# Kernel tuning notes

Measured on AMD Instinct MI355X. Metric: run time of the kernel, lower is better.

The kernel has to match this reference:

```python
import jax, jax.numpy as jnp
import numpy as np

B, L, D = 64, 512, 768          # batch, BERT seq len, BERT hidden
J = 31                          # clause boundaries per doc
S = J + 1                       # clauses per doc (= decoder max_len)
H = 100                         # enc/dec GRU hidden
NC = 10                         # num label classes
EMB = 50                        # label embedding dim


def setup_inputs() -> dict:
    key = jax.random.key(0)
    ks = jax.random.split(key, 24)
    sc = 0.05
    hidden_state = jax.random.normal(ks[0], (B, L, D), jnp.float32)
    # strictly increasing, non-zero boundaries -> every clause slice is non-empty
    stride = L // S  # 16
    bert_clause_b = jnp.tile(((jnp.arange(J) + 1) * stride)[None, :], (B, 1)).astype(jnp.int32)
    p = dict(
        hidden_state=hidden_state,
        bert_clause_b=bert_clause_b,
        fc5_w=sc * jax.random.normal(ks[1], (D, 1), jnp.float32),
        fc5_b=jnp.zeros((1,), jnp.float32),
        # encoder bi-GRU (input 768 -> hidden 100), torch gate order r,z,n
        enc_wih_f=sc * jax.random.normal(ks[2], (3 * H, D), jnp.float32),
        enc_whh_f=sc * jax.random.normal(ks[3], (3 * H, H), jnp.float32),
        enc_bih_f=jnp.zeros((3 * H,), jnp.float32),
        enc_bhh_f=jnp.zeros((3 * H,), jnp.float32),
        enc_wih_b=sc * jax.random.normal(ks[4], (3 * H, D), jnp.float32),
        enc_whh_b=sc * jax.random.normal(ks[5], (3 * H, H), jnp.float32),
        enc_bih_b=jnp.zeros((3 * H,), jnp.float32),
        enc_bhh_b=jnp.zeros((3 * H,), jnp.float32),
        emb=sc * jax.random.normal(ks[6], (NC, EMB), jnp.float32),
        lin1_w=sc * jax.random.normal(ks[7], (H, 2 * H), jnp.float32),
        lin1_b=jnp.zeros((H,), jnp.float32),
        dec_wih=sc * jax.random.normal(ks[8], (3 * H, EMB + H), jnp.float32),
        dec_whh=sc * jax.random.normal(ks[9], (3 * H, H), jnp.float32),
        dec_bih=jnp.zeros((3 * H,), jnp.float32),
        dec_bhh=jnp.zeros((3 * H,), jnp.float32),
        h2l_w=sc * jax.random.normal(ks[10], (NC, H), jnp.float32),
        h2l_b=jnp.zeros((NC,), jnp.float32),
    )
    return p


def _gru_cell(x, h, wih, whh, bih, bhh):
    gi = x @ wih.T + bih
    gh = h @ whh.T + bhh
    gir, giz, gin = jnp.split(gi, 3, axis=-1)
    ghr, ghz, ghn = jnp.split(gh, 3, axis=-1)
    r = jax.nn.sigmoid(gir + ghr)
    z = jax.nn.sigmoid(giz + ghz)
    n = jnp.tanh(gin + r * ghn)
    return (1.0 - z) * n + z * h


def _gru_scan(xs, h0, wih, whh, bih, bhh):
    # xs: [T, B, I]
    def step(h, x):
        h2 = _gru_cell(x, h, wih, whh, bih, bhh)
        return h2, h2
    return jax.lax.scan(step, h0, xs)


def reference(hidden_state, bert_clause_b, fc5_w, fc5_b,
              enc_wih_f, enc_whh_f, enc_bih_f, enc_bhh_f,
              enc_wih_b, enc_whh_b, enc_bih_b, enc_bhh_b,
              emb, lin1_w, lin1_b, dec_wih, dec_whh, dec_bih, dec_bhh,
              h2l_w, h2l_b):
    # ---- batched_index_select: per-clause softmax-weighted pooling ----
    t = jnp.arange(L)
    seg_id = jnp.sum(t[None, :, None] >= bert_clause_b[:, None, :], axis=-1)  # [B, L]
    scores = jnp.squeeze(hidden_state @ fc5_w, -1) + fc5_b[0]                  # [B, L]
    mask = seg_id[:, None, :] == jnp.arange(S)[None, :, None]                  # [B, S, L]
    logits = jnp.where(mask, scores[:, None, :], -jnp.inf)
    w = jax.nn.softmax(logits, axis=-1)                                        # [B, S, L]
    doc = jnp.einsum('bsl,bld->bsd', w, hidden_state)                          # [B, S, D]

    # ---- encoder bi-GRU ----
    xs = doc.transpose(1, 0, 2)  # [S, B, D]
    h0 = jnp.zeros((B, H), jnp.float32)
    hT_f, ys_f = _gru_scan(xs, h0, enc_wih_f, enc_whh_f, enc_bih_f, enc_bhh_f)
    _, ys_b = _gru_scan(xs[::-1], h0, enc_wih_b, enc_whh_b, enc_bih_b, enc_bhh_b)
    output1 = jnp.concatenate([ys_f, ys_b[::-1]], axis=-1)  # [S, B, 2H]

    # ---- decoder (greedy / testing=True path) ----
    lin = output1 @ lin1_w.T + lin1_b  # [S, B, H]

    def dec_step(carry, lin_t):
        h, prev = carry
        x = jnp.concatenate([emb[prev], lin_t], axis=-1)  # [B, EMB+H]
        h2 = _gru_cell(x, h, dec_wih, dec_whh, dec_bih, dec_bhh)
        logp = jax.nn.log_softmax(h2 @ h2l_w.T + h2l_b, axis=-1)  # [B, NC]
        nxt = jnp.argmax(logp, axis=-1).astype(jnp.int32)
        return (h2, nxt), logp

    init = (hT_f, jnp.zeros((B,), jnp.int32))
    _, outputs = jax.lax.scan(dec_step, init, lin)
    return outputs  # [S, B, NC] log-probs
```

## Files before the change

kernel.cpp:

```cpp
#include <hip/hip_runtime.h>
#include <hip/hip_bf16.h>
#include <math.h>

#define B_ 64
#define L_ 512
#define D_ 768
#define J_ 31
#define S_ 32
#define H_ 100
#define G3 300
#define NC_ 10
#define EMB_ 50
#define OP_ 224

__device__ __forceinline__ float sigmoidf_(float x) { return 1.0f / (1.0f + __expf(-x)); }
__device__ __forceinline__ float tanhf_(float x) {
    float e = __expf(2.0f * x);
    return 1.0f - 2.0f / (e + 1.0f);
}
__device__ __forceinline__ float dot4f_(float4 a, float4 b) {
    return a.x * b.x + a.y * b.y + a.z * b.z + a.w * b.w;
}

typedef _Float16 half2_t __attribute__((ext_vector_type(2)));
typedef _Float16 f16x8 __attribute__((ext_vector_type(8)));
typedef float f32x4 __attribute__((ext_vector_type(4)));
__device__ __forceinline__ half2_t u_as_h2(unsigned u) { return __builtin_bit_cast(half2_t, u); }
__device__ __forceinline__ unsigned packh2(float a, float b) {
    half2_t p; p.x = (_Float16)a; p.y = (_Float16)b;
    return __builtin_bit_cast(unsigned, p);
}

__global__ __launch_bounds__(256) void pool_prep_kernel(
    const float* __restrict__ hs, const int* __restrict__ cb,
    const float* __restrict__ fc5w, const float* __restrict__ fc5b,
    _Float16* __restrict__ doc_h,
    const float* __restrict__ dwih, const float* __restrict__ l1w,
    const float* __restrict__ l1b, const float* __restrict__ emb,
    const float* __restrict__ bih,
    _Float16* __restrict__ W2h, float* __restrict__ b2, float* __restrict__ tcg,
    const float* __restrict__ ewhf, const float* __restrict__ ewhb,
    const float* __restrict__ dwhh, unsigned* __restrict__ wpack,
    const float* __restrict__ ewif, const float* __restrict__ ewib,
    _Float16* __restrict__ wh, _Float16* __restrict__ out1h)
{
    __shared__ __align__(16) float acc_s[4][D_];
    __shared__ float m_s[4], l_s[4];

    int bidx = blockIdx.x;
    int tid = threadIdx.x;

    if (bidx >= 2048) {
        if (bidx < 2348) {
            int n = bidx - 2048;
            __shared__ float dw_s[H_];
            int k = tid;
            if (k < H_) dw_s[k] = dwih[(size_t)n * 150 + 50 + k];
            __syncthreads();
            if (k < 200) {
                float acc = 0.f;
                for (int i = 0; i < H_; ++i) acc += dw_s[i] * l1w[(size_t)i * 200 + k];
                W2h[(size_t)n * OP_ + k] = (_Float16)acc;
            } else if (k == 200) {
                float acc = 0.f;
                for (int i = 0; i < H_; ++i) acc += dw_s[i] * l1b[i];
                b2[n] = acc;
            } else if (k < 211) {
                int c = k - 201;
                float acc = bih[n];
                const float* er = emb + c * EMB_;
                const float* wr = dwih + (size_t)n * 150;
                for (int e = 0; e < EMB_; ++e) acc += er[e] * wr[e];
                tcg[c * G3 + n] = acc;
            } else if (k < 235) {
                W2h[(size_t)n * OP_ + (k - 11)] = (_Float16)0.f;
            }
        } else if (bidx < 2351) {
            int m = bidx - 2348;
            const float* whh = (m == 0) ? ewhf : (m == 1) ? ewhb : dwhh;
            for (int t = tid; t < 400; t += 256) {
                int j = t >> 2, q = t & 3;
                unsigned* o = wpack + (size_t)m * 16000 + (size_t)t * 40;
#pragma unroll
                for (int d = 0; d < 13; ++d) {
                    int k = 2 * (13 * q + d);
                    float r0 = (k < H_) ? whh[j * H_ + k] : 0.f;
                    float r1 = (k + 1 < H_) ? whh[j * H_ + k + 1] : 0.f;
                    float z0 = (k < H_) ? whh[(100 + j) * H_ + k] : 0.f;
                    float z1 = (k + 1 < H_) ? whh[(100 + j) * H_ + k + 1] : 0.f;
                    float n0 = (k < H_) ? whh[(200 + j) * H_ + k] : 0.f;
                    float n1 = (k + 1 < H_) ? whh[(200 + j) * H_ + k + 1] : 0.f;
                    o[d]      = packh2(r0, r1);
                    o[13 + d] = packh2(z0, z1);
                    o[26 + d] = packh2(n0, n1);
                }
                o[39] = 0u;
            }
        } else if (bidx < 2503) {
            int ri = bidx - 2351;
            for (int idx = tid; idx < 3072; idx += 256) {
                int rr = idx / 768;
                int k = idx - rr * 768;
                int n = 4 * ri + rr;
                float v = 0.f;
                if (n < G3) v = ewif[(size_t)n * D_ + k];
                else if (n < 600) v = ewib[(size_t)(n - G3) * D_ + k];
                wh[(size_t)n * D_ + k] = (_Float16)v;
            }
        } else if (bidx < 2511) {
            int r0 = (bidx - 2503) * 256 + tid;
            _Float16* row = out1h + (size_t)r0 * OP_;
            for (int c = 200; c < OP_; ++c) row[c] = (_Float16)0.f;
        } else {
            for (int idx = tid; idx < 4 * OP_; idx += 256) {
                int r = 300 + idx / OP_, c = idx % OP_;
                W2h[(size_t)r * OP_ + c] = (_Float16)0.f;
            }
        }
        return;
    }

    int s = bidx >> 6, b = bidx & 63;
    int start = (s == 0) ? 0 : cb[b * J_ + s - 1];
    int end   = (s == J_) ? L_ : cb[b * J_ + s];
    int nt = end - start;
    int lane = tid & 63, wv = tid >> 6;

    if (nt <= 0) {
        for (int d = tid; d < D_; d += 256) doc_h[((size_t)s * B_ + b) * D_ + d] = (_Float16)0.f;
        return;
    }

    float4 fwv[3];
#pragma unroll
    for (int i = 0; i < 3; ++i)
        fwv[i] = *(const float4*)(fc5w + 4 * lane + 256 * i);
    float bias = fc5b[0];

    const float* base = hs + ((size_t)b * L_ + start) * D_;
    float m = -INFINITY, l = 0.f;
    float4 acc[3];
#pragma unroll
    for (int i = 0; i < 3; ++i) acc[i] = make_float4(0.f, 0.f, 0.f, 0.f);

    for (int t = wv; t < nt; t += 4) {
        const float* row = base + (size_t)t * D_;
        float4 x0 = *(const float4*)(row + 4 * lane);
        float4 x1 = *(const float4*)(row + 4 * lane + 256);
        float4 x2 = *(const float4*)(row + 4 * lane + 512);
        float p = dot4f_(x0, fwv[0]) + dot4f_(x1, fwv[1]) + dot4f_(x2, fwv[2]);
#pragma unroll
        for (int off = 32; off; off >>= 1) p += __shfl_xor(p, off);
        p += bias;
        if (p > m) {
            float sc = __expf(m - p);
            l *= sc;
#pragma unroll
            for (int i = 0; i < 3; ++i) {
                acc[i].x *= sc; acc[i].y *= sc; acc[i].z *= sc; acc[i].w *= sc;
            }
            m = p;
        }
        float e = __expf(p - m);
        l += e;
        acc[0].x += e * x0.x; acc[0].y += e * x0.y; acc[0].z += e * x0.z; acc[0].w += e * x0.w;
        acc[1].x += e * x1.x; acc[1].y += e * x1.y; acc[1].z += e * x1.z; acc[1].w += e * x1.w;
        acc[2].x += e * x2.x; acc[2].y += e * x2.y; acc[2].z += e * x2.z; acc[2].w += e * x2.w;
    }
#pragma unroll
    for (int i = 0; i < 3; ++i)
        *(float4*)&acc_s[wv][4 * lane + 256 * i] = acc[i];
    if (lane == 0) { m_s[wv] = m; l_s[wv] = l; }
    __syncthreads();

    float M = fmaxf(fmaxf(m_s[0], m_s[1]), fmaxf(m_s[2], m_s[3]));
    float f0 = (l_s[0] > 0.f) ? __expf(m_s[0] - M) : 0.f;
    float f1 = (l_s[1] > 0.f) ? __expf(m_s[1] - M) : 0.f;
    float f2 = (l_s[2] > 0.f) ? __expf(m_s[2] - M) : 0.f;
    float f3 = (l_s[3] > 0.f) ? __expf(m_s[3] - M) : 0.f;
    float inv = 1.f / (l_s[0] * f0 + l_s[1] * f1 + l_s[2] * f2 + l_s[3] * f3);
    _Float16* o = doc_h + ((size_t)s * B_ + b) * D_;
#pragma unroll
    for (int i = 0; i < 3; ++i) {
        int d = tid + 256 * i;
        float num = acc_s[0][d] * f0 + acc_s[1][d] * f1
                  + acc_s[2][d] * f2 + acc_s[3][d] * f3;
        o[d] = (_Float16)(num * inv);
    }
}

__global__ __launch_bounds__(256) void gemm_enc_mfma(
    const _Float16* __restrict__ dh, const _Float16* __restrict__ wh,
    const float* __restrict__ bf_, const float* __restrict__ bb_,
    float* __restrict__ C)
{
    int w = threadIdx.x >> 6, l = threadIdx.x & 63;
    int m0 = (blockIdx.y * 4 + w) * 16;
    int n0 = blockIdx.x * 16;
    int rowA = m0 + (l & 15);
    int rowB = n0 + (l & 15);
    int kb = (l >> 4) * 8;

    const f16x8* ap = (const f16x8*)(dh + (size_t)rowA * D_ + kb);
    const f16x8* bp = (const f16x8*)(wh + (size_t)rowB * D_ + kb);
    f32x4 acc = {0.f, 0.f, 0.f, 0.f};
#pragma unroll
    for (int k = 0; k < 24; ++k) {
        f16x8 a = ap[k * 4];
        f16x8 b = bp[k * 4];
        acc = __builtin_amdgcn_mfma_f32_16x16x32_f16(a, b, acc, 0, 0, 0);
    }
    int nc = n0 + (l & 15);
    if (nc < 600) {
        float bias = (nc < G3) ? bf_[nc] : bb_[nc - G3];
#pragma unroll
        for (int r = 0; r < 4; ++r) {
            int mr = m0 + (l >> 4) * 4 + r;
            C[(size_t)mr * 600 + nc] = acc[r] + bias;
        }
    }
}

__global__ __launch_bounds__(256) void gemm_gil_mfma(
    const _Float16* __restrict__ oh, const _Float16* __restrict__ W2h,
    const float* __restrict__ b2, float* __restrict__ C)
{
    int w = threadIdx.x >> 6, l = threadIdx.x & 63;
    int m0 = (blockIdx.y * 4 + w) * 16;
    int n0 = blockIdx.x * 16;
    const f16x8* ap = (const f16x8*)(oh + (size_t)(m0 + (l & 15)) * OP_ + (l >> 4) * 8);
    const f16x8* bp = (const f16x8*)(W2h + (size_t)(n0 + (l & 15)) * OP_ + (l >> 4) * 8);
    f32x4 acc = {0.f, 0.f, 0.f, 0.f};
#pragma unroll
    for (int k = 0; k < 7; ++k) {
        f16x8 a = ap[k * 4];
        f16x8 b = bp[k * 4];
        acc = __builtin_amdgcn_mfma_f32_16x16x32_f16(a, b, acc, 0, 0, 0);
    }
    int nc = n0 + (l & 15);
    if (nc < G3) {
        float bias = b2[nc];
#pragma unroll
        for (int r = 0; r < 4; ++r) {
            int mr = m0 + (l >> 4) * 4 + r;
            C[(size_t)mr * G3 + nc] = acc[r] + bias;
        }
    }
}

#define LOAD_WREGS(WPBASE)                                                  \
    uint4 wq[10];                                                           \
    if (mv) {                                                               \
        const uint4* wp_ = (const uint4*)((WPBASE) + (size_t)tid * 40);     \
        _Pragma("unroll")                                                   \
        for (int i = 0; i < 10; ++i) wq[i] = wp_[i];                        \
    }

#define WD(i) (((i) & 3) == 0 ? wq[(i) >> 2].x : ((i) & 3) == 1 ? wq[(i) >> 2].y \
             : ((i) & 3) == 2 ? wq[(i) >> 2].z : wq[(i) >> 2].w)

#define MATVEC_REG(PBUF)                                                    \
    {                                                                       \
        const unsigned* hh = (const unsigned*)(PBUF);                       \
        _Pragma("unroll")                                                   \
        for (int d = 0; d < 13; ++d) {                                      \
            half2_t hv = u_as_h2(hh[13 * q + d]);                           \
            ar = __builtin_amdgcn_fdot2(u_as_h2(WD(d)),      hv, ar, false); \
            az = __builtin_amdgcn_fdot2(u_as_h2(WD(13 + d)), hv, az, false); \
            an = __builtin_amdgcn_fdot2(u_as_h2(WD(26 + d)), hv, an, false); \
        }                                                                   \
        ar += __shfl_xor(ar, 1); ar += __shfl_xor(ar, 2);                   \
        az += __shfl_xor(az, 1); az += __shfl_xor(az, 2);                   \
        an += __shfl_xor(an, 1); an += __shfl_xor(an, 2);                   \
    }

#define ENCT 448
#define ENC_SUB(GA0, GA1, GA2, NB0, NB1, NB2, SC, SN)                       \
    {                                                                       \
        if (mv) {                                                           \
            if (q == 0 && (SN) < S_) {                                      \
                int tn_ = bwd ? (S_ - 1 - (SN)) : (SN);                     \
                const float* gg_ = gi + ((size_t)tn_ * B_ + b) * 600 + goff; \
                NB0 = gg_[j]; NB1 = gg_[100 + j]; NB2 = gg_[200 + j];       \
            }                                                               \
            float ar = 0.f, az = 0.f, an = 0.f;                             \
            MATVEC_REG(hhalf[p])                                            \
            if (q == 0) {                                                   \
                int tc_ = bwd ? (S_ - 1 - (SC)) : (SC);                     \
                float r = sigmoidf_(GA0 + ar + bhr);                        \
                float z = sigmoidf_(GA1 + az + bhz);                        \
                float n = tanhf_(GA2 + r * (an + bhn));                     \
                float hn = (1.f - z) * n + z * hc;                          \
                hc = hn;                                                    \
                hhalf[p ^ 1][j] = (_Float16)hn;                             \
                out1h[((size_t)tc_ * B_ + b) * OP_ + ooff + j] = (_Float16)hn; \
            }                                                               \
        }                                                                   \
        __syncthreads();                                                    \
        p ^= 1;                                                             \
    }

__global__ __launch_bounds__(ENCT, 1) void enc_scan(
    const float* __restrict__ gi, const unsigned* __restrict__ wpack,
    const float* __restrict__ bhh_f, const float* __restrict__ bhh_b,
    _Float16* __restrict__ out1h, float* __restrict__ hT)
{
    __shared__ __align__(8) _Float16 hhalf[2][104];

    int bid = blockIdx.x;
    int b = bid & 63;
    bool bwd = (bid >= 64);
    const float* bhh = bwd ? bhh_b : bhh_f;
    int tid = threadIdx.x;
    int j = tid >> 2, q = tid & 3;
    bool mv = tid < 400;
    const int goff = bwd ? G3 : 0;
    const int ooff = bwd ? H_ : 0;

    if (tid < 104) { hhalf[0][tid] = (_Float16)0.f; hhalf[1][tid] = (_Float16)0.f; }
    LOAD_WREGS(wpack + (bwd ? 16000 : 0))
    float bhr = 0.f, bhz = 0.f, bhn = 0.f, hc = 0.f;
    float pA0 = 0.f, pA1 = 0.f, pA2 = 0.f, pB0 = 0.f, pB1 = 0.f, pB2 = 0.f;
    if (mv && q == 0) {
        bhr = bhh[j]; bhz = bhh[100 + j]; bhn = bhh[200 + j];
        int t0 = bwd ? (S_ - 1) : 0;
        const float* gg = gi + ((size_t)t0 * B_ + b) * 600 + goff;
        pA0 = gg[j]; pA1 = gg[100 + j]; pA2 = gg[200 + j];
    }
    __syncthreads();

    int p = 0;
    for (int step = 0; step < S_; step += 2) {
        ENC_SUB(pA0, pA1, pA2, pB0, pB1, pB2, step, step + 1)
        ENC_SUB(pB0, pB1, pB2, pA0, pA1, pA2, step + 1, step + 2)
    }
    if (!bwd && mv && q == 0) hT[b * H_ + j] = hc;
}

#define DECT 448
#define DEC_LOGITS(TPREV)                                                   \
    {                                                                       \
        float acc_ = 0.f;                                                   \
        if (lane < 40) {                                                    \
            int c_ = lane >> 2, part_ = lane & 3;                           \
            const float* hr_ = hl_s + c_ * H_;                              \
            const float* hv_ = hf[p];                                       \
            int k0_ = 25 * part_;                                           \
            for (int k_ = k0_; k_ < k0_ + 25; ++k_) acc_ += hr_[k_] * hv_[k_]; \
            acc_ += __shfl_xor(acc_, 1);                                    \
            acc_ += __shfl_xor(acc_, 2);                                    \
        }                                                                   \
        float src_ = __shfl(acc_, (lane < NC_) ? 4 * lane : 0);             \
        float lv_ = (lane < NC_) ? src_ + hlb_r : -INFINITY;                \
        float mx_ = lv_; int am_ = lane & 15;                               \
        _Pragma("unroll")                                                   \
        for (int m_ = 8; m_; m_ >>= 1) {                                    \
            float ov_ = __shfl_xor(mx_, m_);                                \
            int oa_ = __shfl_xor(am_, m_);                                  \
            if (ov_ > mx_ || (ov_ == mx_ && oa_ < am_)) { mx_ = ov_; am_ = oa_; } \
        }                                                                   \
        if (w0) {                                                           \
            float e_ = (lane < NC_) ? __expf(lv_ - mx_) : 0.f;              \
            float se_ = e_;                                                 \
            _Pragma("unroll")                                               \
            for (int m_ = 8; m_; m_ >>= 1) se_ += __shfl_xor(se_, m_);      \
            if (lane < NC_) {                                               \
                float lse_ = mx_ + __logf(se_);                             \
                out[((size_t)(TPREV) * B_ + b) * NC_ + lane] = lv_ - lse_;  \
            }                                                               \
        }                                                                   \
        prev = __shfl(am_, 0);                                              \
    }

#define DEC_SUB(GA0, GA1, GA2, NB0, NB1, NB2, TC)                           \
    {                                                                       \
        float ar = 0.f, az = 0.f, an = 0.f;                                 \
        if (mv && (TC) < S_) {                                              \
            if (q == 0 && (TC) + 1 < S_) {                                  \
                const float* gg_ = gi_lin + ((size_t)((TC) + 1) * B_ + b) * G3; \
                NB0 = gg_[j]; NB1 = gg_[100 + j]; NB2 = gg_[200 + j];       \
            }                                                               \
            MATVEC_REG(hhalf[p])                                            \
        }                                                                   \
        if ((TC) >= 1) DEC_LOGITS((TC) - 1)                                 \
        if (mv && (TC) < S_ && q == 0) {                                    \
            const float* tcp_ = tc_s + prev * G3;                           \
            float r = sigmoidf_(GA0 + tcp_[j]       + ar + bhr);            \
            float z = sigmoidf_(GA1 + tcp_[100 + j] + az + bhz);            \
            float n = tanhf_(   GA2 + tcp_[200 + j] + r * (an + bhn));      \
            float hn = (1.f - z) * n + z * hc;                              \
            hc = hn;                                                        \
            hf[p ^ 1][j] = hn;                                              \
            hhalf[p ^ 1][j] = (_Float16)hn;                                 \
        }                                                                   \
        __syncthreads();                                                    \
        p ^= 1;                                                             \
    }

__global__ __launch_bounds__(DECT, 1) void dec_scan(
    const float* __restrict__ gi_lin, const unsigned* __restrict__ wpack,
    const float* __restrict__ bhh, const float* __restrict__ tcg,
    const float* __restrict__ h2lw, const float* __restrict__ h2lb,
    const float* __restrict__ hT, float* __restrict__ out)
{
    __shared__ float tc_s[NC_ * G3];
    __shared__ float hl_s[NC_ * H_];
    __shared__ __align__(8) _Float16 hhalf[2][104];
    __shared__ __align__(16) float hf[2][104];

    int bid = blockIdx.x;
    int b = bid & 63;
    int tid = threadIdx.x;
    int j = tid >> 2, q = tid & 3;
    bool mv = tid < 400;
    int lane = tid & 63;
    bool w0 = (tid < 64);

    for (int idx = tid; idx < NC_ * G3; idx += DECT) tc_s[idx] = tcg[idx];
    for (int idx = tid; idx < NC_ * H_; idx += DECT) hl_s[idx] = h2lw[idx];
    if (tid < 104) {
        float hv = (tid < H_) ? hT[b * H_ + tid] : 0.f;
        hf[0][tid] = hv;            hf[1][tid] = 0.f;
        hhalf[0][tid] = (_Float16)hv; hhalf[1][tid] = (_Float16)0.f;
    }
    LOAD_WREGS(wpack + 32000)
    float bhr = 0.f, bhz = 0.f, bhn = 0.f, hc = 0.f;
    float pA0 = 0.f, pA1 = 0.f, pA2 = 0.f, pB0 = 0.f, pB1 = 0.f, pB2 = 0.f;
    if (mv && q == 0) {
        bhr = bhh[j]; bhz = bhh[100 + j]; bhn = bhh[200 + j];
        hc = hT[b * H_ + j];
        const float* gg = gi_lin + ((size_t)0 * B_ + b) * G3;
        pA0 = gg[j]; pA1 = gg[100 + j]; pA2 = gg[200 + j];
    }
    float hlb_r = (lane < NC_) ? h2lb[lane] : 0.f;
    int prev = 0;
    __syncthreads();

    int p = 0;
    DEC_SUB(pA0, pA1, pA2, pB0, pB1, pB2, 0)
    for (int it = 0; it < 16; ++it) {
        int tA = 2 * it + 1, tB = 2 * it + 2;
        DEC_SUB(pB0, pB1, pB2, pA0, pA1, pA2, tA)
        DEC_SUB(pA0, pA1, pA2, pB0, pB1, pB2, tB)
    }
}

extern "C" void kernel_launch(void* const* d_in, const int* in_sizes, int n_in,
                              void* d_out, int out_size, void* d_ws, size_t ws_size,
                              hipStream_t stream)
{
    const float* hs   = (const float*)d_in[0];
    const int*   cb   = (const int*)  d_in[1];
    const float* fc5w = (const float*)d_in[2];
    const float* fc5b = (const float*)d_in[3];
    const float* ewif = (const float*)d_in[4];
    const float* ewhf = (const float*)d_in[5];
    const float* ebif = (const float*)d_in[6];
    const float* ebhf = (const float*)d_in[7];
    const float* ewib = (const float*)d_in[8];
    const float* ewhb = (const float*)d_in[9];
    const float* ebib = (const float*)d_in[10];
    const float* ebhb = (const float*)d_in[11];
    const float* emb  = (const float*)d_in[12];
    const float* l1w  = (const float*)d_in[13];
    const float* l1b  = (const float*)d_in[14];
    const float* dwih = (const float*)d_in[15];
    const float* dwhh = (const float*)d_in[16];
    const float* dbih = (const float*)d_in[17];
    const float* dbhh = (const float*)d_in[18];
    const float* h2lw = (const float*)d_in[19];
    const float* h2lb = (const float*)d_in[20];
    float* out = (float*)d_out;

    float* ws   = (float*)d_ws;
    _Float16* doc_h = (_Float16*)ws;
    _Float16* wh    = (_Float16*)(ws + 800000);
    float* gi    = ws + 1572864;
    _Float16* out1h = (_Float16*)(gi + 1228800);
    float* hT    = gi + 1228800 + 230000;
    float* b2    = hT + 6400;
    float* tcg   = b2 + 320;
    float* gil   = tcg + 3072;
    unsigned* wpack = (unsigned*)(gil + 614400);
    _Float16* W2h = (_Float16*)(wpack + 48000);

    pool_prep_kernel<<<2512, 256, 0, stream>>>(
        hs, cb, fc5w, fc5b, doc_h,
        dwih, l1w, l1b, emb, dbih, W2h, b2, tcg,
        ewhf, ewhb, dwhh, wpack,
        ewif, ewib, wh, out1h);
    gemm_enc_mfma<<<dim3(38, 32), 256, 0, stream>>>(doc_h, wh, ebif, ebib, gi);
    enc_scan<<<128, ENCT, 0, stream>>>(gi, wpack, ebhf, ebhb, out1h, hT);
    gemm_gil_mfma<<<dim3(19, 32), 256, 0, stream>>>(out1h, W2h, b2, gil);
    dec_scan<<<64, DECT, 0, stream>>>(gil, wpack, dbhh, tcg,
                                      h2lw, h2lb, hT, out);
}
```

Measured before the change: 144.2 us.

## Fuse input-projection GEMMs into encoder and decoder scan kernels via shared memory

Removes the two standalone MFMA GEMM kernels. Each scan block now computes its own per-batch input projections (32 timesteps by 300 gates) with MFMA into shared memory before the recurrence. This cuts two kernel launches and the global round trip of the gi/gil intermediates. In exchange, the per-batch GEMM runs on only 128 or 64 blocks instead of a wide grid, which makes the scan prologue longer, and the software prefetch of gate inputs is replaced by shared-memory reads.

```diff
diff --git a/kernel.cpp b/kernel.cpp
--- a/kernel.cpp
+++ b/kernel.cpp
@@ -189,65 +189,6 @@
     }
 }
 
-__global__ __launch_bounds__(256) void gemm_enc_mfma(
-    const _Float16* __restrict__ dh, const _Float16* __restrict__ wh,
-    const float* __restrict__ bf_, const float* __restrict__ bb_,
-    float* __restrict__ C)
-{
-    int w = threadIdx.x >> 6, l = threadIdx.x & 63;
-    int m0 = (blockIdx.y * 4 + w) * 16;
-    int n0 = blockIdx.x * 16;
-    int rowA = m0 + (l & 15);
-    int rowB = n0 + (l & 15);
-    int kb = (l >> 4) * 8;
-
-    const f16x8* ap = (const f16x8*)(dh + (size_t)rowA * D_ + kb);
-    const f16x8* bp = (const f16x8*)(wh + (size_t)rowB * D_ + kb);
-    f32x4 acc = {0.f, 0.f, 0.f, 0.f};
-#pragma unroll
-    for (int k = 0; k < 24; ++k) {
-        f16x8 a = ap[k * 4];
-        f16x8 b = bp[k * 4];
-        acc = __builtin_amdgcn_mfma_f32_16x16x32_f16(a, b, acc, 0, 0, 0);
-    }
-    int nc = n0 + (l & 15);
-    if (nc < 600) {
-        float bias = (nc < G3) ? bf_[nc] : bb_[nc - G3];
-#pragma unroll
-        for (int r = 0; r < 4; ++r) {
-            int mr = m0 + (l >> 4) * 4 + r;
-            C[(size_t)mr * 600 + nc] = acc[r] + bias;
-        }
-    }
-}
-
-__global__ __launch_bounds__(256) void gemm_gil_mfma(
-    const _Float16* __restrict__ oh, const _Float16* __restrict__ W2h,
-    const float* __restrict__ b2, float* __restrict__ C)
-{
-    int w = threadIdx.x >> 6, l = threadIdx.x & 63;
-    int m0 = (blockIdx.y * 4 + w) * 16;
-    int n0 = blockIdx.x * 16;
-    const f16x8* ap = (const f16x8*)(oh + (size_t)(m0 + (l & 15)) * OP_ + (l >> 4) * 8);
-    const f16x8* bp = (const f16x8*)(W2h + (size_t)(n0 + (l & 15)) * OP_ + (l >> 4) * 8);
-    f32x4 acc = {0.f, 0.f, 0.f, 0.f};
-#pragma unroll
-    for (int k = 0; k < 7; ++k) {
-        f16x8 a = ap[k * 4];
-        f16x8 b = bp[k * 4];
-        acc = __builtin_amdgcn_mfma_f32_16x16x32_f16(a, b, acc, 0, 0, 0);
-    }
-    int nc = n0 + (l & 15);
-    if (nc < G3) {
-        float bias = b2[nc];
-#pragma unroll
-        for (int r = 0; r < 4; ++r) {
-            int mr = m0 + (l >> 4) * 4 + r;
-            C[(size_t)mr * G3 + nc] = acc[r] + bias;
-        }
-    }
-}
-
 #define LOAD_WREGS(WPBASE)                                                  \
     uint4 wq[10];                                                           \
     if (mv) {                                                               \
@@ -275,64 +216,73 @@
     }
 
 #define ENCT 448
-#define ENC_SUB(GA0, GA1, GA2, NB0, NB1, NB2, SC, SN)                       \
-    {                                                                       \
-        if (mv) {                                                           \
-            if (q == 0 && (SN) < S_) {                                      \
-                int tn_ = bwd ? (S_ - 1 - (SN)) : (SN);                     \
-                const float* gg_ = gi + ((size_t)tn_ * B_ + b) * 600 + goff; \
-                NB0 = gg_[j]; NB1 = gg_[100 + j]; NB2 = gg_[200 + j];       \
-            }                                                               \
-            float ar = 0.f, az = 0.f, an = 0.f;                             \
-            MATVEC_REG(hhalf[p])                                            \
-            if (q == 0) {                                                   \
-                int tc_ = bwd ? (S_ - 1 - (SC)) : (SC);                     \
-                float r = sigmoidf_(GA0 + ar + bhr);                        \
-                float z = sigmoidf_(GA1 + az + bhz);                        \
-                float n = tanhf_(GA2 + r * (an + bhn));                     \
-                float hn = (1.f - z) * n + z * hc;                          \
-                hc = hn;                                                    \
-                hhalf[p ^ 1][j] = (_Float16)hn;                             \
-                out1h[((size_t)tc_ * B_ + b) * OP_ + ooff + j] = (_Float16)hn; \
-            }                                                               \
-        }                                                                   \
-        __syncthreads();                                                    \
-        p ^= 1;                                                             \
-    }
-
 __global__ __launch_bounds__(ENCT, 1) void enc_scan(
-    const float* __restrict__ gi, const unsigned* __restrict__ wpack,
+    const _Float16* __restrict__ doc_h, const _Float16* __restrict__ wh,
+    const float* __restrict__ bih_f, const float* __restrict__ bih_b,
+    const unsigned* __restrict__ wpack,
     const float* __restrict__ bhh_f, const float* __restrict__ bhh_b,
     _Float16* __restrict__ out1h, float* __restrict__ hT)
 {
+    __shared__ __align__(16) float gis[S_][304];
     __shared__ __align__(8) _Float16 hhalf[2][104];
 
     int bid = blockIdx.x;
     int b = bid & 63;
     bool bwd = (bid >= 64);
     const float* bhh = bwd ? bhh_b : bhh_f;
+    const float* bii = bwd ? bih_b : bih_f;
     int tid = threadIdx.x;
     int j = tid >> 2, q = tid & 3;
     bool mv = tid < 400;
     const int goff = bwd ? G3 : 0;
     const int ooff = bwd ? H_ : 0;
+    int w = tid >> 6, l = tid & 63;
 
     if (tid < 104) { hhalf[0][tid] = (_Float16)0.f; hhalf[1][tid] = (_Float16)0.f; }
     LOAD_WREGS(wpack + (bwd ? 16000 : 0))
     float bhr = 0.f, bhz = 0.f, bhn = 0.f, hc = 0.f;
-    float pA0 = 0.f, pA1 = 0.f, pA2 = 0.f, pB0 = 0.f, pB1 = 0.f, pB2 = 0.f;
-    if (mv && q == 0) {
-        bhr = bhh[j]; bhz = bhh[100 + j]; bhn = bhh[200 + j];
-        int t0 = bwd ? (S_ - 1) : 0;
-        const float* gg = gi + ((size_t)t0 * B_ + b) * 600 + goff;
-        pA0 = gg[j]; pA1 = gg[100 + j]; pA2 = gg[200 + j];
+    if (mv && q == 0) { bhr = bhh[j]; bhz = bhh[100 + j]; bhn = bhh[200 + j]; }
+
+    for (int tt = w; tt < 38; tt += 7) {
+        int mt = tt & 1, nt = tt >> 1;
+        int trow = mt * 16 + (l & 15);
+        const f16x8* ap = (const f16x8*)(doc_h + ((size_t)trow * B_ + b) * D_ + (l >> 4) * 8);
+        int rowB = goff + nt * 16 + (l & 15);
+        const f16x8* bp = (const f16x8*)(wh + (size_t)rowB * D_ + (l >> 4) * 8);
+        f32x4 acc = {0.f, 0.f, 0.f, 0.f};
+#pragma unroll
+        for (int k = 0; k < 24; ++k)
+            acc = __builtin_amdgcn_mfma_f32_16x16x32_f16(ap[k * 4], bp[k * 4], acc, 0, 0, 0);
+        int ncl = nt * 16 + (l & 15);
+        float bias = (ncl < G3) ? bii[ncl] : 0.f;
+#pragma unroll
+        for (int r = 0; r < 4; ++r) {
+            int mr = mt * 16 + (l >> 4) * 4 + r;
+            gis[mr][ncl] = acc[r] + bias;
+        }
     }
     __syncthreads();
 
     int p = 0;
-    for (int step = 0; step < S_; step += 2) {
-        ENC_SUB(pA0, pA1, pA2, pB0, pB1, pB2, step, step + 1)
-        ENC_SUB(pB0, pB1, pB2, pA0, pA1, pA2, step + 1, step + 2)
+    for (int step = 0; step < S_; ++step) {
+        int t = bwd ? (S_ - 1 - step) : step;
+        if (mv) {
+            float ga0 = 0.f, ga1 = 0.f, ga2 = 0.f;
+            if (q == 0) { ga0 = gis[t][j]; ga1 = gis[t][100 + j]; ga2 = gis[t][200 + j]; }
+            float ar = 0.f, az = 0.f, an = 0.f;
+            MATVEC_REG(hhalf[p])
+            if (q == 0) {
+                float r = sigmoidf_(ga0 + ar + bhr);
+                float z = sigmoidf_(ga1 + az + bhz);
+                float n = tanhf_(ga2 + r * (an + bhn));
+                float hn = (1.f - z) * n + z * hc;
+                hc = hn;
+                hhalf[p ^ 1][j] = (_Float16)hn;
+                out1h[((size_t)t * B_ + b) * OP_ + ooff + j] = (_Float16)hn;
+            }
+        }
+        __syncthreads();
+        p ^= 1;
     }
     if (!bwd && mv && q == 0) hT[b * H_ + j] = hc;
 }
@@ -372,37 +322,14 @@
         prev = __shfl(am_, 0);                                              \
     }
 
-#define DEC_SUB(GA0, GA1, GA2, NB0, NB1, NB2, TC)                           \
-    {                                                                       \
-        float ar = 0.f, az = 0.f, an = 0.f;                                 \
-        if (mv && (TC) < S_) {                                              \
-            if (q == 0 && (TC) + 1 < S_) {                                  \
-                const float* gg_ = gi_lin + ((size_t)((TC) + 1) * B_ + b) * G3; \
-                NB0 = gg_[j]; NB1 = gg_[100 + j]; NB2 = gg_[200 + j];       \
-            }                                                               \
-            MATVEC_REG(hhalf[p])                                            \
-        }                                                                   \
-        if ((TC) >= 1) DEC_LOGITS((TC) - 1)                                 \
-        if (mv && (TC) < S_ && q == 0) {                                    \
-            const float* tcp_ = tc_s + prev * G3;                           \
-            float r = sigmoidf_(GA0 + tcp_[j]       + ar + bhr);            \
-            float z = sigmoidf_(GA1 + tcp_[100 + j] + az + bhz);            \
-            float n = tanhf_(   GA2 + tcp_[200 + j] + r * (an + bhn));      \
-            float hn = (1.f - z) * n + z * hc;                              \
-            hc = hn;                                                        \
-            hf[p ^ 1][j] = hn;                                              \
-            hhalf[p ^ 1][j] = (_Float16)hn;                                 \
-        }                                                                   \
-        __syncthreads();                                                    \
-        p ^= 1;                                                             \
-    }
-
 __global__ __launch_bounds__(DECT, 1) void dec_scan(
-    const float* __restrict__ gi_lin, const unsigned* __restrict__ wpack,
+    const _Float16* __restrict__ out1h, const _Float16* __restrict__ W2h,
+    const float* __restrict__ b2, const unsigned* __restrict__ wpack,
     const float* __restrict__ bhh, const float* __restrict__ tcg,
     const float* __restrict__ h2lw, const float* __restrict__ h2lb,
     const float* __restrict__ hT, float* __restrict__ out)
 {
+    __shared__ __align__(16) float gils[S_][304];
     __shared__ float tc_s[NC_ * G3];
     __shared__ float hl_s[NC_ * H_];
     __shared__ __align__(8) _Float16 hhalf[2][104];
@@ -415,6 +342,7 @@
     bool mv = tid < 400;
     int lane = tid & 63;
     bool w0 = (tid < 64);
+    int w = tid >> 6, l = tid & 63;
 
     for (int idx = tid; idx < NC_ * G3; idx += DECT) tc_s[idx] = tcg[idx];
     for (int idx = tid; idx < NC_ * H_; idx += DECT) hl_s[idx] = h2lw[idx];
@@ -425,23 +353,54 @@
     }
     LOAD_WREGS(wpack + 32000)
     float bhr = 0.f, bhz = 0.f, bhn = 0.f, hc = 0.f;
-    float pA0 = 0.f, pA1 = 0.f, pA2 = 0.f, pB0 = 0.f, pB1 = 0.f, pB2 = 0.f;
     if (mv && q == 0) {
         bhr = bhh[j]; bhz = bhh[100 + j]; bhn = bhh[200 + j];
         hc = hT[b * H_ + j];
-        const float* gg = gi_lin + ((size_t)0 * B_ + b) * G3;
-        pA0 = gg[j]; pA1 = gg[100 + j]; pA2 = gg[200 + j];
     }
     float hlb_r = (lane < NC_) ? h2lb[lane] : 0.f;
     int prev = 0;
+
+    for (int tt = w; tt < 38; tt += 7) {
+        int mt = tt & 1, nt = tt >> 1;
+        int trow = mt * 16 + (l & 15);
+        const f16x8* ap = (const f16x8*)(out1h + ((size_t)trow * B_ + b) * OP_ + (l >> 4) * 8);
+        int rowB = nt * 16 + (l & 15);
+        const f16x8* bp = (const f16x8*)(W2h + (size_t)rowB * OP_ + (l >> 4) * 8);
+        f32x4 acc = {0.f, 0.f, 0.f, 0.f};
+#pragma unroll
+        for (int k = 0; k < 7; ++k)
+            acc = __builtin_amdgcn_mfma_f32_16x16x32_f16(ap[k * 4], bp[k * 4], acc, 0, 0, 0);
+        int ncl = nt * 16 + (l & 15);
+        float bias = (ncl < G3) ? b2[ncl] : 0.f;
+#pragma unroll
+        for (int r = 0; r < 4; ++r) {
+            int mr = mt * 16 + (l >> 4) * 4 + r;
+            gils[mr][ncl] = acc[r] + bias;
+        }
+    }
     __syncthreads();
 
     int p = 0;
-    DEC_SUB(pA0, pA1, pA2, pB0, pB1, pB2, 0)
-    for (int it = 0; it < 16; ++it) {
-        int tA = 2 * it + 1, tB = 2 * it + 2;
-        DEC_SUB(pB0, pB1, pB2, pA0, pA1, pA2, tA)
-        DEC_SUB(pA0, pA1, pA2, pB0, pB1, pB2, tB)
+    for (int t = 0; t <= S_; ++t) {
+        float ar = 0.f, az = 0.f, an = 0.f;
+        float ga0 = 0.f, ga1 = 0.f, ga2 = 0.f;
+        if (mv && t < S_) {
+            if (q == 0) { ga0 = gils[t][j]; ga1 = gils[t][100 + j]; ga2 = gils[t][200 + j]; }
+            MATVEC_REG(hhalf[p])
+        }
+        if (t >= 1) DEC_LOGITS(t - 1)
+        if (mv && t < S_ && q == 0) {
+            const float* tcp_ = tc_s + prev * G3;
+            float r = sigmoidf_(ga0 + tcp_[j]       + ar + bhr);
+            float z = sigmoidf_(ga1 + tcp_[100 + j] + az + bhz);
+            float n = tanhf_(   ga2 + tcp_[200 + j] + r * (an + bhn));
+            float hn = (1.f - z) * n + z * hc;
+            hc = hn;
+            hf[p ^ 1][j] = hn;
+            hhalf[p ^ 1][j] = (_Float16)hn;
+        }
+        __syncthreads();
+        p ^= 1;
     }
 }
 
@@ -475,23 +434,20 @@
     float* ws   = (float*)d_ws;
     _Float16* doc_h = (_Float16*)ws;
     _Float16* wh    = (_Float16*)(ws + 800000);
-    float* gi    = ws + 1572864;
-    _Float16* out1h = (_Float16*)(gi + 1228800);
-    float* hT    = gi + 1228800 + 230000;
-    float* b2    = hT + 6400;
-    float* tcg   = b2 + 320;
-    float* gil   = tcg + 3072;
-    unsigned* wpack = (unsigned*)(gil + 614400);
-    _Float16* W2h = (_Float16*)(wpack + 48000);
+    _Float16* out1h = (_Float16*)(ws + 1100000);
+    float* hT    = ws + 1400000;
+    float* b2    = ws + 1410000;
+    float* tcg   = ws + 1411000;
+    unsigned* wpack = (unsigned*)(ws + 1420000);
+    _Float16* W2h = (_Float16*)(ws + 1470000);
 
     pool_prep_kernel<<<2512, 256, 0, stream>>>(
         hs, cb, fc5w, fc5b, doc_h,
         dwih, l1w, l1b, emb, dbih, W2h, b2, tcg,
         ewhf, ewhb, dwhh, wpack,
         ewif, ewib, wh, out1h);
-    gemm_enc_mfma<<<dim3(38, 32), 256, 0, stream>>>(doc_h, wh, ebif, ebib, gi);
-    enc_scan<<<128, ENCT, 0, stream>>>(gi, wpack, ebhf, ebhb, out1h, hT);
-    gemm_gil_mfma<<<dim3(19, 32), 256, 0, stream>>>(out1h, W2h, b2, gil);
-    dec_scan<<<64, DECT, 0, stream>>>(gil, wpack, dbhh, tcg,
+    enc_scan<<<128, ENCT, 0, stream>>>(doc_h, wh, ebif, ebib, wpack,
+                                       ebhf, ebhb, out1h, hT);
+    dec_scan<<<64, DECT, 0, stream>>>(out1h, W2h, b2, wpack, dbhh, tcg,
                                       h2lw, h2lb, hT, out);
 }
```

New measurement: 169.9 us. +17.8%, slower.
